# Performance work log

Measured on AMD Instinct MI355X. Metric: run time of the kernel, lower is better.

## Reference

```python
import jax, jax.numpy as jnp
import numpy as np

N_NODES = 100000
N_EDGES = 1600000
IN_CH = 128
HID_CH = 128


def setup_inputs() -> dict:
    key = jax.random.key(0)
    ks = jax.random.split(key, 12)
    s = 1.0 / np.sqrt(IN_CH)
    sh = 1.0 / np.sqrt(HID_CH)
    return {
        "x": jax.random.normal(ks[0], (N_NODES, IN_CH), dtype=jnp.float32),
        "edge_index": jax.random.randint(ks[1], (2, N_EDGES), 0, N_NODES, dtype=jnp.int32),
        # SAGEConv1: lin_l (applied to aggregated neighbors, has bias), lin_r (root)
        "W1_l": jax.random.uniform(ks[2], (IN_CH, HID_CH), jnp.float32, -s, s),
        "b1": jax.random.uniform(ks[3], (HID_CH,), jnp.float32, -s, s),
        "W1_r": jax.random.uniform(ks[4], (IN_CH, HID_CH), jnp.float32, -s, s),
        # SAGEConv2
        "W2_l": jax.random.uniform(ks[5], (HID_CH, HID_CH), jnp.float32, -sh, sh),
        "b2": jax.random.uniform(ks[6], (HID_CH,), jnp.float32, -sh, sh),
        "W2_r": jax.random.uniform(ks[7], (HID_CH, HID_CH), jnp.float32, -sh, sh),
        # decoder Linear(hidden, in)
        "Wd": jax.random.uniform(ks[8], (HID_CH, IN_CH), jnp.float32, -sh, sh),
        "bd": jax.random.uniform(ks[9], (IN_CH,), jnp.float32, -sh, sh),
        "alpha": jnp.float32(0.5),
    }


def _sage_conv(h, src, dst, n_nodes, W_l, b, W_r):
    # PyG SAGEConv (mean aggr): out = lin_l(mean_{j in N(i)} x_j) + lin_r(x_i)
    msg = h[src]  # [E, C] gather from source nodes
    agg = jax.ops.segment_sum(msg, dst, num_segments=n_nodes)  # [N, C]
    cnt = jax.ops.segment_sum(jnp.ones((src.shape[0],), h.dtype), dst,
                              num_segments=n_nodes)  # [N]
    mean = agg / jnp.maximum(cnt, 1.0)[:, None]
    return mean @ W_l + b + h @ W_r


def reference(x, edge_index, W1_l, b1, W1_r, W2_l, b2, W2_r, Wd, bd, alpha):
    n_nodes = x.shape[0]
    src, dst = edge_index[0], edge_index[1]
    h = jax.nn.relu(_sage_conv(x, src, dst, n_nodes, W1_l, b1, W1_r))
    # dropout p=0.2 is identity in eval mode
    h = jax.nn.relu(_sage_conv(h, src, dst, n_nodes, W2_l, b2, W2_r))
    x_updated = h @ Wd + bd
    return alpha * x_updated + (1.0 - alpha) * x
```

## Files before the change

### kernel.cpp

```cpp
#include <hip/hip_runtime.h>
#include <cstddef>
#include <cstdint>

#define CH 128
#define NBKT 196
#define ABLK 320
#define BKT_NODES 512
#define BKTCAP 10240

typedef __attribute__((ext_vector_type(8))) short short8;
typedef __attribute__((ext_vector_type(4))) float f32x4;

__device__ __forceinline__ unsigned short f2bf(float f) {
  unsigned u = __float_as_uint(f);
  u += 0x7FFF + ((u >> 16) & 1);
  return (unsigned short)(u >> 16);
}
__device__ __forceinline__ float bf_lo(unsigned int u) {
  return __uint_as_float(u << 16);
}
__device__ __forceinline__ float bf_hi(unsigned int u) {
  return __uint_as_float(u & 0xffff0000u);
}
__device__ __forceinline__ void gld16(const void* g, void* l) {
  __builtin_amdgcn_global_load_lds((const __attribute__((address_space(1))) unsigned int*)g,
                                   (__attribute__((address_space(3))) unsigned int*)l, 16, 0, 0);
}

__global__ __launch_bounds__(1024)
void k_prebin(const int* __restrict__ src, const int* __restrict__ dst,
              int* __restrict__ cnt, unsigned int* __restrict__ binned,
              int E, int chunk,
              const float4* __restrict__ in, uint4* __restrict__ out, int n8,
              const float* __restrict__ w0, const float* __restrict__ w1,
              const float* __restrict__ w2, const float* __restrict__ w3,
              const float* __restrict__ w4, unsigned short* __restrict__ wdst) {
  __shared__ int c[NBKT];
  __shared__ int curq[NBKT];
  int b = blockIdx.x;
  int t = threadIdx.x;
  if (b < ABLK) {
    for (int i = t; i < NBKT; i += 1024) c[i] = 0;
    __syncthreads();
    int s = b * chunk;
    int e = min(s + chunk, E);
    for (int i = s + t; i < e; i += 1024)
      atomicAdd(&c[dst[i] >> 9], 1);
    __syncthreads();
    for (int i = t; i < NBKT; i += 1024)
      curq[i] = atomicAdd(&cnt[i], c[i]);
    __syncthreads();
    for (int i = s + t; i < e; i += 1024) {
      int d = dst[i];
      int bb = d >> 9;
      int pos = atomicAdd(&curq[bb], 1);
      binned[(size_t)bb * BKTCAP + pos] = (unsigned)src[i] | ((unsigned)(d & 511) << 17);
    }
  } else if (b < ABLK + 5) {
    const float* srcs[5] = {w0, w1, w2, w3, w4};
    const float* w = srcs[b - ABLK];
    unsigned short* d = wdst + (size_t)(b - ABLK) * CH * CH;
    for (int idx = t; idx < CH * CH; idx += 1024) {
      int k = idx >> 7, nn = idx & 127;
      d[nn * CH + k] = f2bf(w[idx]);
    }
  } else {
    int i = (b - ABLK - 5) * 1024 + t;
    if (i < n8) {
      float4 a = in[i * 2], cc = in[i * 2 + 1];
      uint4 o;
      o.x = (unsigned)f2bf(a.x) | ((unsigned)f2bf(a.y) << 16);
      o.y = (unsigned)f2bf(a.z) | ((unsigned)f2bf(a.w) << 16);
      o.z = (unsigned)f2bf(cc.x) | ((unsigned)f2bf(cc.y) << 16);
      o.w = (unsigned)f2bf(cc.z) | ((unsigned)f2bf(cc.w) << 16);
      out[i] = o;
    }
  }
}

__global__ __launch_bounds__(1024)
void k_bucket(const unsigned int* __restrict__ binned, const int* __restrict__ cnt,
              int* __restrict__ rowptr, int* __restrict__ sorted, int N, int E, int nbkt) {
  __shared__ int c[BKT_NODES];
  __shared__ int tsum[256];
  __shared__ int cur[BKT_NODES];
  __shared__ int bscan[256];
  int b = blockIdx.x, t = threadIdx.x;
  int cv = 0;
  if (t < 256) { cv = (t < nbkt) ? cnt[t] : 0; bscan[t] = cv; }
  __syncthreads();
  for (int o = 1; o < 256; o <<= 1) {
    int y = 0;
    if (t < 256 && t >= o) y = bscan[t - o];
    __syncthreads();
    if (t < 256) bscan[t] += y;
    __syncthreads();
  }
  int cntb = cnt[b];
  int gbase = bscan[b] - cntb;
  size_t sread = (size_t)b * BKTCAP;

  if (t < BKT_NODES) c[t] = 0;
  __syncthreads();
  for (int i = t; i < cntb; i += 1024)
    atomicAdd(&c[binned[sread + i] >> 17], 1);
  __syncthreads();
  int v0 = 0, v1 = 0, tot = 0;
  if (t < 256) { v0 = c[2 * t]; v1 = c[2 * t + 1]; tot = v0 + v1; tsum[t] = tot; }
  __syncthreads();
  for (int o = 1; o < 256; o <<= 1) {
    int y = 0;
    if (t < 256 && t >= o) y = tsum[t - o];
    __syncthreads();
    if (t < 256) tsum[t] += y;
    __syncthreads();
  }
  if (t < 256) {
    int excl = tsum[t] - tot;
    int base = b * BKT_NODES;
    int r0 = gbase + excl, r1 = gbase + excl + v0;
    if (base + 2 * t < N)     rowptr[base + 2 * t]     = r0;
    if (base + 2 * t + 1 < N) rowptr[base + 2 * t + 1] = r1;
    cur[2 * t] = r0; cur[2 * t + 1] = r1;
  }
  __syncthreads();
  for (int i = t; i < cntb; i += 1024) {
    unsigned w = binned[sread + i];
    int pos = atomicAdd(&cur[w >> 17], 1);
    sorted[pos] = w & 0x1FFFF;
  }
  if (b == nbkt - 1 && t == 0) rowptr[N] = E;
}

__global__ __launch_bounds__(256)
void k_agg(const uint4* __restrict__ in4, uint4* __restrict__ out4,
           const int* __restrict__ rowptr, const int* __restrict__ sorted_src,
           int n, int nwaves) {
  int wid = (blockIdx.x * 256 + threadIdx.x) >> 6;
  int lane = threadIdx.x & 63;
  int quad = lane >> 4;
  int sl = lane & 15;

  for (int node = wid; node < n; node += nwaves) {
    int beg = rowptr[node], end = rowptr[node + 1];
    float a0 = 0.f, a1 = 0.f, a2 = 0.f, a3 = 0.f;
    float a4 = 0.f, a5 = 0.f, a6 = 0.f, a7 = 0.f;
    int e = beg;
    for (; e + 16 <= end; e += 16) {
      uint4 v[4];
#pragma unroll
      for (int j = 0; j < 4; j++)
        v[j] = in4[((unsigned)sorted_src[e + 4 * j + quad] << 4) + sl];
#pragma unroll
      for (int j = 0; j < 4; j++) {
        a0 += bf_lo(v[j].x); a1 += bf_hi(v[j].x);
        a2 += bf_lo(v[j].y); a3 += bf_hi(v[j].y);
        a4 += bf_lo(v[j].z); a5 += bf_hi(v[j].z);
        a6 += bf_lo(v[j].w); a7 += bf_hi(v[j].w);
      }
    }
    if (e < end) {
      uint4 v[4];
#pragma unroll
      for (int j = 0; j < 4; j++) {
        int k = e + 4 * j + quad;
        int idx = (k < end) ? k : beg;
        uint4 tv = in4[((unsigned)sorted_src[idx] << 4) + sl];
        if (k >= end) { tv.x = 0u; tv.y = 0u; tv.z = 0u; tv.w = 0u; }
        v[j] = tv;
      }
#pragma unroll
      for (int j = 0; j < 4; j++) {
        a0 += bf_lo(v[j].x); a1 += bf_hi(v[j].x);
        a2 += bf_lo(v[j].y); a3 += bf_hi(v[j].y);
        a4 += bf_lo(v[j].z); a5 += bf_hi(v[j].z);
        a6 += bf_lo(v[j].w); a7 += bf_hi(v[j].w);
      }
    }
    a0 += __shfl(a0, lane ^ 16); a1 += __shfl(a1, lane ^ 16);
    a2 += __shfl(a2, lane ^ 16); a3 += __shfl(a3, lane ^ 16);
    a4 += __shfl(a4, lane ^ 16); a5 += __shfl(a5, lane ^ 16);
    a6 += __shfl(a6, lane ^ 16); a7 += __shfl(a7, lane ^ 16);
    a0 += __shfl(a0, lane ^ 32); a1 += __shfl(a1, lane ^ 32);
    a2 += __shfl(a2, lane ^ 32); a3 += __shfl(a3, lane ^ 32);
    a4 += __shfl(a4, lane ^ 32); a5 += __shfl(a5, lane ^ 32);
    a6 += __shfl(a6, lane ^ 32); a7 += __shfl(a7, lane ^ 32);
    int d = end - beg;
    float inv = (d > 0) ? (1.f / (float)d) : 0.f;
    if (quad == 0) {
      uint4 o;
      o.x = (unsigned)f2bf(a0 * inv) | ((unsigned)f2bf(a1 * inv) << 16);
      o.y = (unsigned)f2bf(a2 * inv) | ((unsigned)f2bf(a3 * inv) << 16);
      o.z = (unsigned)f2bf(a4 * inv) | ((unsigned)f2bf(a5 * inv) << 16);
      o.w = (unsigned)f2bf(a6 * inv) | ((unsigned)f2bf(a7 * inv) << 16);
      out4[((unsigned)node << 4) + sl] = o;
    }
  }
}

__global__ __launch_bounds__(256, 2)
void k_sage(const unsigned short* __restrict__ Am, const unsigned short* __restrict__ Ax,
            const unsigned short* __restrict__ WTl, const unsigned short* __restrict__ WTr,
            const float* __restrict__ bias, unsigned short* __restrict__ out, int n) {
  __shared__ unsigned short sA[128 * 64];
  __shared__ unsigned short sB[128 * 64];
  int tid = threadIdx.x;
  int lane = tid & 63;
  int w = tid >> 6;
  int row0 = blockIdx.x * 128;
  int col_lo = lane & 15, quad = lane >> 4;
  int rx = col_lo & 7;

  f32x4 acc[2][8];
#pragma unroll
  for (int mt = 0; mt < 2; mt++)
#pragma unroll
    for (int nt = 0; nt < 8; nt++) acc[mt][nt] = (f32x4){0.f, 0.f, 0.f, 0.f};

  const unsigned short* As[4] = {Am, Am, Ax, Ax};
  const unsigned short* Bs[4] = {WTl, WTl, WTr, WTr};
  const int k0s[4] = {0, 64, 0, 64};

  for (int c = 0; c < 4; c++) {
    const unsigned short* Ap = As[c];
    const unsigned short* Bp = Bs[c];
    int k0 = k0s[c];
#pragma unroll
    for (int it = 0; it < 4; it++) {
      int flat = it * 256 + tid;
      int r = flat >> 3;
      int sl8 = flat & 7;
      int kof = (sl8 ^ (r & 7)) * 8;
      int gr = row0 + r;
      if (gr > n - 1) gr = n - 1;
      gld16(Ap + (size_t)gr * CH + k0 + kof, sA + flat * 8);
      gld16(Bp + (size_t)r * CH + k0 + kof, sB + flat * 8);
    }
    __syncthreads();

#pragma unroll
    for (int ks = 0; ks < 2; ks++) {
      int so = ((ks * 4 + quad) ^ rx) * 8;
      short8 a0 = *(const short8*)&sA[(w * 32 + col_lo) * 64 + so];
      short8 a1 = *(const short8*)&sA[(w * 32 + 16 + col_lo) * 64 + so];
      short8 b[8];
#pragma unroll
      for (int nt = 0; nt < 8; nt++)
        b[nt] = *(const short8*)&sB[(nt * 16 + col_lo) * 64 + so];
#pragma unroll
      for (int nt = 0; nt < 8; nt++) {
        acc[0][nt] = __builtin_amdgcn_mfma_f32_16x16x32_bf16(a0, b[nt], acc[0][nt], 0, 0, 0);
        acc[1][nt] = __builtin_amdgcn_mfma_f32_16x16x32_bf16(a1, b[nt], acc[1][nt], 0, 0, 0);
      }
    }
    __syncthreads();
  }

#pragma unroll
  for (int nt = 0; nt < 8; nt++) {
    float bb = bias[nt * 16 + col_lo];
#pragma unroll
    for (int mt = 0; mt < 2; mt++) {
#pragma unroll
      for (int r = 0; r < 4; r++) {
        int rr = row0 + w * 32 + mt * 16 + quad * 4 + r;
        if (rr < n) {
          float v = fmaxf(acc[mt][nt][r] + bb, 0.f);
          out[(size_t)rr * CH + nt * 16 + col_lo] = f2bf(v);
        }
      }
    }
  }
}

__global__ __launch_bounds__(256, 2)
void k_dec(const unsigned short* __restrict__ H, const unsigned short* __restrict__ WTd,
           const float* __restrict__ bd, const float* __restrict__ X,
           const float* __restrict__ alpha_p, float* __restrict__ out, int n) {
  __shared__ unsigned short sA[128 * 64];
  __shared__ unsigned short sB[128 * 64];
  int tid = threadIdx.x;
  int lane = tid & 63;
  int w = tid >> 6;
  int row0 = blockIdx.x * 128;
  int col_lo = lane & 15, quad = lane >> 4;
  int rx = col_lo & 7;

  f32x4 acc[2][8];
#pragma unroll
  for (int mt = 0; mt < 2; mt++)
#pragma unroll
    for (int nt = 0; nt < 8; nt++) acc[mt][nt] = (f32x4){0.f, 0.f, 0.f, 0.f};

  for (int c = 0; c < 2; c++) {
    int k0 = c * 64;
#pragma unroll
    for (int it = 0; it < 4; it++) {
      int flat = it * 256 + tid;
      int r = flat >> 3;
      int sl8 = flat & 7;
      int kof = (sl8 ^ (r & 7)) * 8;
      int gr = row0 + r;
      if (gr > n - 1) gr = n - 1;
      gld16(H + (size_t)gr * CH + k0 + kof, sA + flat * 8);
      gld16(WTd + (size_t)r * CH + k0 + kof, sB + flat * 8);
    }
    __syncthreads();

#pragma unroll
    for (int ks = 0; ks < 2; ks++) {
      int so = ((ks * 4 + quad) ^ rx) * 8;
      short8 a0 = *(const short8*)&sA[(w * 32 + col_lo) * 64 + so];
      short8 a1 = *(const short8*)&sA[(w * 32 + 16 + col_lo) * 64 + so];
      short8 b[8];
#pragma unroll
      for (int nt = 0; nt < 8; nt++)
        b[nt] = *(const short8*)&sB[(nt * 16 + col_lo) * 64 + so];
#pragma unroll
      for (int nt = 0; nt < 8; nt++) {
        acc[0][nt] = __builtin_amdgcn_mfma_f32_16x16x32_bf16(a0, b[nt], acc[0][nt], 0, 0, 0);
        acc[1][nt] = __builtin_amdgcn_mfma_f32_16x16x32_bf16(a1, b[nt], acc[1][nt], 0, 0, 0);
      }
    }
    __syncthreads();
  }

  float al = alpha_p[0];
  float be = 1.f - al;
#pragma unroll
  for (int nt = 0; nt < 8; nt++) {
    float bb = bd[nt * 16 + col_lo];
#pragma unroll
    for (int mt = 0; mt < 2; mt++) {
#pragma unroll
      for (int r = 0; r < 4; r++) {
        int rr = row0 + w * 32 + mt * 16 + quad * 4 + r;
        if (rr < n) {
          int cc = nt * 16 + col_lo;
          float xv = X[(size_t)rr * CH + cc];
          out[(size_t)rr * CH + cc] = al * (acc[mt][nt][r] + bb) + be * xv;
        }
      }
    }
  }
}


extern "C" void kernel_launch(void* const* d_in, const int* in_sizes, int n_in,
                              void* d_out, int out_size, void* d_ws, size_t ws_size,
                              hipStream_t stream) {
  const float* x   = (const float*)d_in[0];
  const int*   ei  = (const int*)d_in[1];
  const float* W1l = (const float*)d_in[2];
  const float* b1  = (const float*)d_in[3];
  const float* W1r = (const float*)d_in[4];
  const float* W2l = (const float*)d_in[5];
  const float* b2  = (const float*)d_in[6];
  const float* W2r = (const float*)d_in[7];
  const float* Wd  = (const float*)d_in[8];
  const float* bd  = (const float*)d_in[9];
  const float* alp = (const float*)d_in[10];

  int N = in_sizes[0] / CH;
  int E = in_sizes[1] / 2;
  const int* src = ei;
  const int* dst = ei + E;

  char* ws = (char*)d_ws;
  size_t off = 0;
  auto alloc = [&](size_t bytes) -> char* {
    off = (off + 511) & ~size_t(511);
    char* p = ws + off;
    off += bytes;
    return p;
  };
  int*   rowptr = (int*)alloc((size_t)(N + 1) * 4);
  int*   cnt    = (int*)alloc((size_t)NBKT * 4);
  int*   sorted = (int*)alloc((size_t)E * 4);
  unsigned short* xb = (unsigned short*)alloc((size_t)N * CH * 2);
  unsigned short* h  = (unsigned short*)alloc((size_t)N * CH * 2);
  unsigned short* WT = (unsigned short*)alloc((size_t)5 * CH * CH * 2);
  unsigned short* mean = (unsigned short*)d_out;
  unsigned int* binned = (unsigned int*)((char*)d_out + (size_t)N * CH * 2);

  int chunk = (E + ABLK - 1) / ABLK;
  int n8 = N * CH / 8;
  int gCvt = (n8 + 1023) / 1024;

  hipMemsetAsync(cnt, 0, (size_t)NBKT * 4, stream);
  k_prebin<<<ABLK + 5 + gCvt, 1024, 0, stream>>>(src, dst, cnt, binned, E, chunk,
                                                 (const float4*)x, (uint4*)xb, n8,
                                                 W1l, W1r, W2l, W2r, Wd, WT);
  k_bucket<<<NBKT, 1024, 0, stream>>>(binned, cnt, rowptr, sorted, N, E, NBKT);

  int gAggBlocks = 6144;
  int nWaves = gAggBlocks * 4;
  int gGemm = (N + 127) / 128;
  unsigned short* WT1l = WT + 0 * CH * CH;
  unsigned short* WT1r = WT + 1 * CH * CH;
  unsigned short* WT2l = WT + 2 * CH * CH;
  unsigned short* WT2r = WT + 3 * CH * CH;
  unsigned short* WTd  = WT + 4 * CH * CH;

  k_agg<<<gAggBlocks, 256, 0, stream>>>((const uint4*)xb, (uint4*)mean, rowptr, sorted, N, nWaves);
  k_sage<<<gGemm, 256, 0, stream>>>(mean, xb, WT1l, WT1r, b1, h, N);
  k_agg<<<gAggBlocks, 256, 0, stream>>>((const uint4*)h, (uint4*)mean, rowptr, sorted, N, nWaves);
  k_sage<<<gGemm, 256, 0, stream>>>(mean, h, WT2l, WT2r, b2, h, N);
  k_dec<<<gGemm, 256, 0, stream>>>(h, WTd, bd, x, alp, (float*)d_out, N);
}
```

Before: 350.3 us.

## Fuse neighbor mean aggregation into SAGE GEMM kernel via shared-memory staging

Replaces the separate aggregation and SAGE GEMM kernels with one per-layer kernel. Each block gathers and averages neighbor features for its 128 rows directly into swizzled LDS tiles, then runs the lin_l and lin_r MFMA products. This removes the global write and re-read of the mean buffer and one launch per layer. The gather phase now runs with far fewer resident waves than the former 6144-block aggregation grid, which may reduce memory-level parallelism for the random gathers.

Measured after the change: 464.0 us. 1.32x slower.

```diff
diff --git a/kernel.cpp b/kernel.cpp
--- a/kernel.cpp
+++ b/kernel.cpp
@@ -132,49 +132,74 @@
   if (b == nbkt - 1 && t == 0) rowptr[N] = E;
 }
 
-__global__ __launch_bounds__(256)
-void k_agg(const uint4* __restrict__ in4, uint4* __restrict__ out4,
-           const int* __restrict__ rowptr, const int* __restrict__ sorted_src,
-           int n, int nwaves) {
-  int wid = (blockIdx.x * 256 + threadIdx.x) >> 6;
-  int lane = threadIdx.x & 63;
-  int quad = lane >> 4;
+__global__ __launch_bounds__(256, 2)
+void k_layer(const uint4* __restrict__ in4,
+             const unsigned short* __restrict__ Ax,
+             const int* __restrict__ rowptr, const int* __restrict__ sorted_src,
+             const unsigned short* __restrict__ WTl, const unsigned short* __restrict__ WTr,
+             const float* __restrict__ bias, unsigned short* __restrict__ out, int n) {
+  __shared__ unsigned short sA0[128 * 64];
+  __shared__ unsigned short sA1[128 * 64];
+  __shared__ unsigned short sB0[128 * 64];
+  __shared__ unsigned short sB1[128 * 64];
+  int tid = threadIdx.x;
+  int lane = tid & 63;
+  int w = tid >> 6;
+  int row0 = blockIdx.x * 128;
+  int col_lo = lane & 15, quad = lane >> 4;
+  int rx = col_lo & 7;
   int sl = lane & 15;
 
-  for (int node = wid; node < n; node += nwaves) {
-    int beg = rowptr[node], end = rowptr[node + 1];
+#pragma unroll
+  for (int it = 0; it < 4; it++) {
+    int flat = it * 256 + tid;
+    int r = flat >> 3;
+    int sl8 = flat & 7;
+    int kof = (sl8 ^ (r & 7)) * 8;
+    gld16(WTl + (size_t)r * CH + 0 + kof, sB0 + flat * 8);
+    gld16(WTl + (size_t)r * CH + 64 + kof, sB1 + flat * 8);
+  }
+
+  for (int i = 0; i < 32; i++) {
+    int lr = w * 32 + i;
+    int node = row0 + lr;
     float a0 = 0.f, a1 = 0.f, a2 = 0.f, a3 = 0.f;
     float a4 = 0.f, a5 = 0.f, a6 = 0.f, a7 = 0.f;
-    int e = beg;
-    for (; e + 16 <= end; e += 16) {
-      uint4 v[4];
-#pragma unroll
-      for (int j = 0; j < 4; j++)
-        v[j] = in4[((unsigned)sorted_src[e + 4 * j + quad] << 4) + sl];
-#pragma unroll
-      for (int j = 0; j < 4; j++) {
-        a0 += bf_lo(v[j].x); a1 += bf_hi(v[j].x);
-        a2 += bf_lo(v[j].y); a3 += bf_hi(v[j].y);
-        a4 += bf_lo(v[j].z); a5 += bf_hi(v[j].z);
-        a6 += bf_lo(v[j].w); a7 += bf_hi(v[j].w);
-      }
-    }
-    if (e < end) {
-      uint4 v[4];
-#pragma unroll
-      for (int j = 0; j < 4; j++) {
-        int k = e + 4 * j + quad;
-        int idx = (k < end) ? k : beg;
-        uint4 tv = in4[((unsigned)sorted_src[idx] << 4) + sl];
-        if (k >= end) { tv.x = 0u; tv.y = 0u; tv.z = 0u; tv.w = 0u; }
-        v[j] = tv;
-      }
-#pragma unroll
-      for (int j = 0; j < 4; j++) {
-        a0 += bf_lo(v[j].x); a1 += bf_hi(v[j].x);
-        a2 += bf_lo(v[j].y); a3 += bf_hi(v[j].y);
-        a4 += bf_lo(v[j].z); a5 += bf_hi(v[j].z);
-        a6 += bf_lo(v[j].w); a7 += bf_hi(v[j].w);
+    int d = 0;
+    if (node < n) {
+      int beg = rowptr[node], end = rowptr[node + 1];
+      d = end - beg;
+      int e = beg;
+      for (; e + 16 <= end; e += 16) {
+        uint4 v[4];
+#pragma unroll
+        for (int j = 0; j < 4; j++)
+          v[j] = in4[((unsigned)sorted_src[e + 4 * j + quad] << 4) + sl];
+#pragma unroll
+        for (int j = 0; j < 4; j++) {
+          a0 += bf_lo(v[j].x); a1 += bf_hi(v[j].x);
+          a2 += bf_lo(v[j].y); a3 += bf_hi(v[j].y);
+          a4 += bf_lo(v[j].z); a5 += bf_hi(v[j].z);
+          a6 += bf_lo(v[j].w); a7 += bf_hi(v[j].w);
+        }
+      }
+      if (e < end) {
+        uint4 v[4];
+#pragma unroll
+        for (int j = 0; j < 4; j++) {
+          int k = e + 4 * j + quad;
+          int idx = (k < end) ? k : beg;
+          uint4 tv = in4[((unsigned)sorted_src[idx] << 4) + sl];
+          if (k >= end) { tv.x = 0u; tv.y = 0u; tv.z = 0u; tv.w = 0u; }
+          v[j] = tv;
+        }
+#pragma unroll
+        for (int j = 0; j < 4; j++) {
+          a0 += bf_lo(v[j].x); a1 += bf_hi(v[j].x);
+          a2 += bf_lo(v[j].y); a3 += bf_hi(v[j].y);
+          a4 += bf_lo(v[j].z); a5 += bf_hi(v[j].z);
+          a6 += bf_lo(v[j].w); a7 += bf_hi(v[j].w);
+        }
       }
     }
     a0 += __shfl(a0, lane ^ 16); a1 += __shfl(a1, lane ^ 16);
@@ -185,7 +210,6 @@
     a2 += __shfl(a2, lane ^ 32); a3 += __shfl(a3, lane ^ 32);
     a4 += __shfl(a4, lane ^ 32); a5 += __shfl(a5, lane ^ 32);
     a6 += __shfl(a6, lane ^ 32); a7 += __shfl(a7, lane ^ 32);
-    int d = end - beg;
     float inv = (d > 0) ? (1.f / (float)d) : 0.f;
     if (quad == 0) {
       uint4 o;
@@ -193,23 +217,11 @@
       o.y = (unsigned)f2bf(a2 * inv) | ((unsigned)f2bf(a3 * inv) << 16);
       o.z = (unsigned)f2bf(a4 * inv) | ((unsigned)f2bf(a5 * inv) << 16);
       o.w = (unsigned)f2bf(a6 * inv) | ((unsigned)f2bf(a7 * inv) << 16);
-      out4[((unsigned)node << 4) + sl] = o;
-    }
-  }
-}
-
-__global__ __launch_bounds__(256, 2)
-void k_sage(const unsigned short* __restrict__ Am, const unsigned short* __restrict__ Ax,
-            const unsigned short* __restrict__ WTl, const unsigned short* __restrict__ WTr,
-            const float* __restrict__ bias, unsigned short* __restrict__ out, int n) {
-  __shared__ unsigned short sA[128 * 64];
-  __shared__ unsigned short sB[128 * 64];
-  int tid = threadIdx.x;
-  int lane = tid & 63;
-  int w = tid >> 6;
-  int row0 = blockIdx.x * 128;
-  int col_lo = lane & 15, quad = lane >> 4;
-  int rx = col_lo & 7;
+      unsigned short* dstL = (sl < 8) ? sA0 : sA1;
+      *(uint4*)&dstL[lr * 64 + ((sl & 7) ^ (lr & 7)) * 8] = o;
+    }
+  }
+  __syncthreads();
 
   f32x4 acc[2][8];
 #pragma unroll
@@ -217,43 +229,62 @@
 #pragma unroll
     for (int nt = 0; nt < 8; nt++) acc[mt][nt] = (f32x4){0.f, 0.f, 0.f, 0.f};
 
-  const unsigned short* As[4] = {Am, Am, Ax, Ax};
-  const unsigned short* Bs[4] = {WTl, WTl, WTr, WTr};
-  const int k0s[4] = {0, 64, 0, 64};
-
-  for (int c = 0; c < 4; c++) {
-    const unsigned short* Ap = As[c];
-    const unsigned short* Bp = Bs[c];
-    int k0 = k0s[c];
-#pragma unroll
-    for (int it = 0; it < 4; it++) {
-      int flat = it * 256 + tid;
-      int r = flat >> 3;
-      int sl8 = flat & 7;
-      int kof = (sl8 ^ (r & 7)) * 8;
-      int gr = row0 + r;
-      if (gr > n - 1) gr = n - 1;
-      gld16(Ap + (size_t)gr * CH + k0 + kof, sA + flat * 8);
-      gld16(Bp + (size_t)r * CH + k0 + kof, sB + flat * 8);
-    }
-    __syncthreads();
-
+#pragma unroll
+  for (int cb = 0; cb < 2; cb++) {
+    const unsigned short* pA = cb ? sA1 : sA0;
+    const unsigned short* pB = cb ? sB1 : sB0;
 #pragma unroll
     for (int ks = 0; ks < 2; ks++) {
       int so = ((ks * 4 + quad) ^ rx) * 8;
-      short8 a0 = *(const short8*)&sA[(w * 32 + col_lo) * 64 + so];
-      short8 a1 = *(const short8*)&sA[(w * 32 + 16 + col_lo) * 64 + so];
+      short8 a0 = *(const short8*)&pA[(w * 32 + col_lo) * 64 + so];
+      short8 a1 = *(const short8*)&pA[(w * 32 + 16 + col_lo) * 64 + so];
       short8 b[8];
 #pragma unroll
       for (int nt = 0; nt < 8; nt++)
-        b[nt] = *(const short8*)&sB[(nt * 16 + col_lo) * 64 + so];
+        b[nt] = *(const short8*)&pB[(nt * 16 + col_lo) * 64 + so];
 #pragma unroll
       for (int nt = 0; nt < 8; nt++) {
         acc[0][nt] = __builtin_amdgcn_mfma_f32_16x16x32_bf16(a0, b[nt], acc[0][nt], 0, 0, 0);
         acc[1][nt] = __builtin_amdgcn_mfma_f32_16x16x32_bf16(a1, b[nt], acc[1][nt], 0, 0, 0);
       }
     }
-    __syncthreads();
+  }
+  __syncthreads();
+
+#pragma unroll
+  for (int it = 0; it < 4; it++) {
+    int flat = it * 256 + tid;
+    int r = flat >> 3;
+    int sl8 = flat & 7;
+    int kof = (sl8 ^ (r & 7)) * 8;
+    int gr = row0 + r;
+    if (gr > n - 1) gr = n - 1;
+    gld16(Ax + (size_t)gr * CH + 0 + kof, sA0 + flat * 8);
+    gld16(Ax + (size_t)gr * CH + 64 + kof, sA1 + flat * 8);
+    gld16(WTr + (size_t)r * CH + 0 + kof, sB0 + flat * 8);
+    gld16(WTr + (size_t)r * CH + 64 + kof, sB1 + flat * 8);
+  }
+  __syncthreads();
+
+#pragma unroll
+  for (int cb = 0; cb < 2; cb++) {
+    const unsigned short* pA = cb ? sA1 : sA0;
+    const unsigned short* pB = cb ? sB1 : sB0;
+#pragma unroll
+    for (int ks = 0; ks < 2; ks++) {
+      int so = ((ks * 4 + quad) ^ rx) * 8;
+      short8 a0 = *(const short8*)&pA[(w * 32 + col_lo) * 64 + so];
+      short8 a1 = *(const short8*)&pA[(w * 32 + 16 + col_lo) * 64 + so];
+      short8 b[8];
+#pragma unroll
+      for (int nt = 0; nt < 8; nt++)
+        b[nt] = *(const short8*)&pB[(nt * 16 + col_lo) * 64 + so];
+#pragma unroll
+      for (int nt = 0; nt < 8; nt++) {
+        acc[0][nt] = __builtin_amdgcn_mfma_f32_16x16x32_bf16(a0, b[nt], acc[0][nt], 0, 0, 0);
+        acc[1][nt] = __builtin_amdgcn_mfma_f32_16x16x32_bf16(a1, b[nt], acc[1][nt], 0, 0, 0);
+      }
+    }
   }
 
 #pragma unroll
@@ -380,8 +411,8 @@
   unsigned short* xb = (unsigned short*)alloc((size_t)N * CH * 2);
   unsigned short* h  = (unsigned short*)alloc((size_t)N * CH * 2);
   unsigned short* WT = (unsigned short*)alloc((size_t)5 * CH * CH * 2);
-  unsigned short* mean = (unsigned short*)d_out;
   unsigned int* binned = (unsigned int*)((char*)d_out + (size_t)N * CH * 2);
+  unsigned short* h2 = xb;
 
   int chunk = (E + ABLK - 1) / ABLK;
   int n8 = N * CH / 8;
@@ -393,8 +424,6 @@
                                                  W1l, W1r, W2l, W2r, Wd, WT);
   k_bucket<<<NBKT, 1024, 0, stream>>>(binned, cnt, rowptr, sorted, N, E, NBKT);
 
-  int gAggBlocks = 6144;
-  int nWaves = gAggBlocks * 4;
   int gGemm = (N + 127) / 128;
   unsigned short* WT1l = WT + 0 * CH * CH;
   unsigned short* WT1r = WT + 1 * CH * CH;
@@ -402,9 +431,9 @@
   unsigned short* WT2r = WT + 3 * CH * CH;
   unsigned short* WTd  = WT + 4 * CH * CH;
 
-  k_agg<<<gAggBlocks, 256, 0, stream>>>((const uint4*)xb, (uint4*)mean, rowptr, sorted, N, nWaves);
-  k_sage<<<gGemm, 256, 0, stream>>>(mean, xb, WT1l, WT1r, b1, h, N);
-  k_agg<<<gAggBlocks, 256, 0, stream>>>((const uint4*)h, (uint4*)mean, rowptr, sorted, N, nWaves);
-  k_sage<<<gGemm, 256, 0, stream>>>(mean, h, WT2l, WT2r, b2, h, N);
-  k_dec<<<gGemm, 256, 0, stream>>>(h, WTd, bd, x, alp, (float*)d_out, N);
-}
+  k_layer<<<gGemm, 256, 0, stream>>>((const uint4*)xb, xb, rowptr, sorted,
+                                     WT1l, WT1r, b1, h, N);
+  k_layer<<<gGemm, 256, 0, stream>>>((const uint4*)h, h, rowptr, sorted,
+                                     WT2l, WT2r, b2, h2, N);
+  k_dec<<<gGemm, 256, 0, stream>>>(h2, WTd, bd, x, alp, (float*)d_out, N);
+}
```
